# Kernel tuning notes

Hardware: AMD Instinct MI355X
Metric: run time of the kernel (lower is better)

The kernel has to match this reference:

```python
import jax, jax.numpy as jnp
import numpy as np
from jax import lax

B, HB, WB, CB = 128, 64, 64, 16      # board batch, height, width, channels
HI, WI, CI = 72, 72, 4               # image size/channels (fixed by module)
HIDC = CB - 4                         # board hidden channels = 12
IMGC = 72                             # img_channel_n
POSTC = IMGC + 4                      # 76
FIRE_RATE = 0.5
BN_EPS = 1e-3                         # keras BatchNormalization default epsilon


def setup_inputs() -> dict:
    key = jax.random.key(0)
    k = jax.random.split(key, 8)
    x = jax.random.normal(k[0], (B, HB, WB, CB), jnp.float32)
    images = jax.random.uniform(k[1], (B, HI, WI, CI), jnp.float32)
    conv1_w = jax.random.normal(k[2], (3, 3, CI, 32), jnp.float32) * (1.0 / np.sqrt(9 * CI))
    conv2_w = jax.random.normal(k[3], (3, 3, 32, 32), jnp.float32) * (1.0 / np.sqrt(9 * 32))
    flat = (HI // 4) * (WI // 4) * 32  # 18*18*32 = 10368 after two 2x2 pools
    dense_w = jax.random.normal(k[4], (flat, HIDC * IMGC), jnp.float32) * (1.0 / np.sqrt(flat))
    upd_w1 = jax.random.normal(k[5], (POSTC * 3, 128), jnp.float32) * (1.0 / np.sqrt(POSTC * 3))
    upd_w2 = jax.random.normal(k[6], (128, CB), jnp.float32) * 0.02
    return dict(
        x=x, images=images,
        bn1_gamma=jnp.ones((CI,), jnp.float32), bn1_beta=jnp.zeros((CI,), jnp.float32),
        bn1_mean=jnp.zeros((CI,), jnp.float32), bn1_var=jnp.ones((CI,), jnp.float32),
        conv1_w=conv1_w, conv1_b=jnp.zeros((32,), jnp.float32),
        bn2_gamma=jnp.ones((32,), jnp.float32), bn2_beta=jnp.zeros((32,), jnp.float32),
        bn2_mean=jnp.zeros((32,), jnp.float32), bn2_var=jnp.ones((32,), jnp.float32),
        conv2_w=conv2_w, conv2_b=jnp.zeros((32,), jnp.float32),
        dense_w=dense_w, dense_b=jnp.zeros((HIDC * IMGC,), jnp.float32),
        upd_w1=upd_w1, upd_b1=jnp.zeros((128,), jnp.float32),
        upd_w2=upd_w2, upd_b2=jnp.zeros((CB,), jnp.float32),
    )


def _bn(x, g, b, m, v):
    return (x - m) * lax.rsqrt(v + BN_EPS) * g + b


def _conv_same(x, w, b):
    return lax.conv_general_dilated(x, w, (1, 1), 'SAME',
                                    dimension_numbers=('NHWC', 'HWIO', 'NHWC')) + b


def _maxpool2(x):
    return lax.reduce_window(x, -jnp.inf, lax.max, (1, 2, 2, 1), (1, 2, 2, 1), 'VALID')


def _living_mask(x):
    alpha = x[..., 3:4]
    return lax.reduce_window(alpha, -jnp.inf, lax.max, (1, 3, 3, 1), (1, 1, 1, 1), 'SAME') > 0.1


def _perception_kernel(c):
    # identity + sobel-x + sobel-y, depthwise with multiplier 3 (channel-major order c*3+m)
    ident = np.zeros((3, 3), np.float32); ident[1, 1] = 1.0
    sx = (np.outer([1, 2, 1], [-1, 0, 1]) / 8.0).astype(np.float32)
    sy = sx.T
    k = np.stack([ident, sx, sy], -1)       # (3,3,3)
    k = np.tile(k, (1, 1, c))                # (3,3,3c)
    return jnp.asarray(k[:, :, None, :])     # HWIO with I=1, O=3c


def reference(x, images, bn1_gamma, bn1_beta, bn1_mean, bn1_var, conv1_w, conv1_b,
              bn2_gamma, bn2_beta, bn2_mean, bn2_var, conv2_w, conv2_b,
              dense_w, dense_b, upd_w1, upd_b1, upd_w2, upd_b2):
    # ---- image model (inference mode: BN uses moving stats, dropout = identity) ----
    h = _bn(images, bn1_gamma, bn1_beta, bn1_mean, bn1_var)
    h = jax.nn.relu(_conv_same(h, conv1_w, conv1_b))
    h = _maxpool2(h)
    h = _bn(h, bn2_gamma, bn2_beta, bn2_mean, bn2_var)
    h = jax.nn.relu(_conv_same(h, conv2_w, conv2_b))
    h = _maxpool2(h)
    h = h.reshape(h.shape[0], -1)
    h = jax.nn.relu(h @ dense_w + dense_b)
    filters = h.reshape(-1, HIDC, IMGC)      # (B, 12, 72): per-sample 1x1 conv filter

    # ---- CA step ----
    pre_life = _living_mask(x)
    board_out = x[..., :4]
    hidden = x[..., 4:]
    # per-batch 1x1 VALID conv == batched channel contraction
    img_conv = jnp.einsum('bhwc,bco->bhwo', hidden, filters)
    img_aware = jnp.concatenate([board_out, img_conv], axis=-1)   # (B,H,W,76)
    kern = _perception_kernel(POSTC)
    perceived = lax.conv_general_dilated(img_aware, kern, (1, 1), 'SAME',
                                         dimension_numbers=('NHWC', 'HWIO', 'NHWC'),
                                         feature_group_count=POSTC)  # (B,H,W,228)
    u = jax.nn.relu(jnp.einsum('bhwc,cd->bhwd', perceived, upd_w1) + upd_b1)
    dx = jnp.einsum('bhwd,de->bhwe', u, upd_w2) + upd_b2
    update_mask = jax.random.uniform(jax.random.key(42), x[..., :1].shape) <= FIRE_RATE
    x = x + dx * update_mask.astype(x.dtype)
    post_life = _living_mask(x)
    living = (pre_life & post_life).astype(x.dtype)
    return x * living
```

## Files before the change

### kernel.cpp

```cpp
#include <hip/hip_runtime.h>

#define BN_EPS 1e-3f

typedef __attribute__((ext_vector_type(8))) short bf16x8;
typedef __attribute__((ext_vector_type(4))) short s16x4;
typedef __attribute__((ext_vector_type(4))) float f32x4;

__device__ __forceinline__ unsigned short f2bf_rne(float f) {
  unsigned u = __float_as_uint(f);
  unsigned r = u + 0x7fffu + ((u >> 16) & 1u);
  return (unsigned short)(r >> 16);
}
__device__ __forceinline__ float bf2f(unsigned short h) {
  return __uint_as_float(((unsigned)h) << 16);
}
__device__ __forceinline__ void split2(float v, unsigned short& h, unsigned short& l) {
  h = f2bf_rne(v);
  l = f2bf_rne(v - bf2f(h));
}
__device__ __forceinline__ void split2t(float v, unsigned short& h, unsigned short& l) {
  unsigned u = __float_as_uint(v);
  float hi = __uint_as_float(u & 0xFFFF0000u);
  h = (unsigned short)(u >> 16);
  l = f2bf_rne(v - hi);
}

__device__ __forceinline__ unsigned rotl32(unsigned v, int n) {
  return (v << n) | (v >> (32 - n));
}

__device__ __forceinline__ float tf42_uniform(unsigned i) {
  unsigned x0 = 0u, x1 = i;
  const unsigned k0 = 0u, k1 = 42u, k2 = 0u ^ 42u ^ 0x1BD11BDAu;
  x0 += k0; x1 += k1;
#define TFR(r) { x0 += x1; x1 = rotl32(x1, r); x1 ^= x0; }
  TFR(13) TFR(15) TFR(26) TFR(6)
  x0 += k1; x1 += k2 + 1u;
  TFR(17) TFR(29) TFR(16) TFR(24)
  x0 += k2; x1 += k0 + 2u;
  TFR(13) TFR(15) TFR(26) TFR(6)
  x0 += k0; x1 += k1 + 3u;
  TFR(17) TFR(29) TFR(16) TFR(24)
  x0 += k1; x1 += k2 + 4u;
  TFR(13) TFR(15) TFR(26) TFR(6)
  x0 += k2; x1 += k0 + 5u;
#undef TFR
  unsigned bits = x0 ^ x1;
  return __uint_as_float((bits >> 9) | 0x3F800000u) - 1.0f;
}

__global__ __launch_bounds__(256) void k_conv1(
    const float* __restrict__ img,
    const float* __restrict__ g1, const float* __restrict__ be1,
    const float* __restrict__ m1, const float* __restrict__ v1,
    const float* __restrict__ w, const float* __restrict__ bias,
    const float* __restrict__ g2, const float* __restrict__ be2,
    const float* __restrict__ m2, const float* __restrict__ v2,
    float* __restrict__ h1) {
  int t = blockIdx.x * 256 + threadIdx.x;
  int ox = t % 36, oy = (t / 36) % 36, b = t / 1296;
  float s1[4], t1[4];
#pragma unroll
  for (int ci = 0; ci < 4; ++ci) {
    float s = g1[ci] / sqrtf(v1[ci] + BN_EPS);
    s1[ci] = s; t1[ci] = be1[ci] - m1[ci] * s;
  }
  float pacc[32];
#pragma unroll
  for (int co = 0; co < 32; ++co) pacc[co] = 0.f;
#pragma unroll
  for (int sy = 0; sy < 2; ++sy)
#pragma unroll
  for (int sx = 0; sx < 2; ++sx) {
    int iy = 2 * oy + sy, ix = 2 * ox + sx;
    float acc[32];
#pragma unroll
    for (int co = 0; co < 32; ++co) acc[co] = bias[co];
    for (int ky = 0; ky < 3; ++ky) {
      int yy = iy + ky - 1; if (yy < 0 || yy >= 72) continue;
      for (int kx = 0; kx < 3; ++kx) {
        int xx = ix + kx - 1; if (xx < 0 || xx >= 72) continue;
        float4 p = *(const float4*)(img + (((size_t)b * 72 + yy) * 72 + xx) * 4);
        float in0 = p.x * s1[0] + t1[0];
        float in1 = p.y * s1[1] + t1[1];
        float in2 = p.z * s1[2] + t1[2];
        float in3 = p.w * s1[3] + t1[3];
        const float* wp = w + (ky * 3 + kx) * 128;
#pragma unroll
        for (int co = 0; co < 32; ++co) acc[co] = fmaf(in0, wp[co], acc[co]);
#pragma unroll
        for (int co = 0; co < 32; ++co) acc[co] = fmaf(in1, wp[32 + co], acc[co]);
#pragma unroll
        for (int co = 0; co < 32; ++co) acc[co] = fmaf(in2, wp[64 + co], acc[co]);
#pragma unroll
        for (int co = 0; co < 32; ++co) acc[co] = fmaf(in3, wp[96 + co], acc[co]);
      }
    }
#pragma unroll
    for (int co = 0; co < 32; ++co)
      pacc[co] = fmaxf(pacc[co], fmaxf(acc[co], 0.f));
  }
#pragma unroll
  for (int co = 0; co < 32; ++co) {
    float s = g2[co] / sqrtf(v2[co] + BN_EPS);
    pacc[co] = pacc[co] * s + (be2[co] - m2[co] * s);
  }
  float* op = h1 + (size_t)t * 32;
#pragma unroll
  for (int c4 = 0; c4 < 8; ++c4) {
    float4 v;
    v.x = pacc[c4 * 4]; v.y = pacc[c4 * 4 + 1];
    v.z = pacc[c4 * 4 + 2]; v.w = pacc[c4 * 4 + 3];
    *(float4*)(op + c4 * 4) = v;
  }
}

__global__ __launch_bounds__(256) void k_prep3(
    const float* __restrict__ w, unsigned short* __restrict__ Wh,
    unsigned short* __restrict__ Wl) {
  int t = blockIdx.x * 256 + threadIdx.x;
  int j = t & 7, l = (t >> 3) & 63, nt = (t >> 9) & 1, tap = t >> 10;
  int ci = ((l >> 4) << 3) + j, co = nt * 16 + (l & 15);
  float v = w[tap * 1024 + ci * 32 + co];
  unsigned short hh, ll;
  split2(v, hh, ll);
  Wh[t] = hh;
  Wl[t] = ll;
}

__global__ __launch_bounds__(256, 3) void k_conv2(
    const float* __restrict__ hin,
    const unsigned short* __restrict__ Wch, const unsigned short* __restrict__ Wcl,
    const float* __restrict__ bias, float* __restrict__ h2) {
  __shared__ __align__(16) unsigned short Lh[12960];
  __shared__ __align__(16) unsigned short Ll[12960];
  int tid = threadIdx.x;
  int b = blockIdx.y;
  int tY = (blockIdx.x / 3) * 16, tX = (blockIdx.x % 3) * 16;
  for (int idx = tid; idx < 2592; idx += 256) {
    int pix = idx >> 3, c4 = idx & 7;
    int ly = pix / 18, lx = pix - ly * 18;
    int gy = tY - 1 + ly, gx = tX - 1 + lx;
    float4 v = {0.f, 0.f, 0.f, 0.f};
    if (gy >= 0 && gy < 36 && gx >= 0 && gx < 36)
      v = *(const float4*)(hin + (((size_t)b * 36 + gy) * 36 + gx) * 32 + c4 * 4);
    unsigned short ha, la, hb, lb, hc, lc, hd, ld;
    split2(v.x, ha, la); split2(v.y, hb, lb);
    split2(v.z, hc, lc); split2(v.w, hd, ld);
    s16x4 vh = {(short)ha, (short)hb, (short)hc, (short)hd};
    s16x4 vl = {(short)la, (short)lb, (short)lc, (short)ld};
    *(s16x4*)(Lh + pix * 40 + c4 * 4) = vh;
    *(s16x4*)(Ll + pix * 40 + c4 * 4) = vl;
  }
  __syncthreads();
  int wv = tid >> 6, lane = tid & 63;
  int lr = lane & 15, lhi = lane >> 4;
  int nt = wv & 1, mrow0 = (wv >> 1) * 8;
  bf16x8 wh[9], wl[9];
#pragma unroll
  for (int tap = 0; tap < 9; ++tap) {
    int base = ((tap * 2 + nt) * 64 + lane) * 8;
    wh[tap] = *(const bf16x8*)(Wch + base);
    wl[tap] = *(const bf16x8*)(Wcl + base);
  }
  f32x4 acc[8];
#pragma unroll
  for (int mt = 0; mt < 8; ++mt) acc[mt] = (f32x4){0.f, 0.f, 0.f, 0.f};
#pragma unroll
  for (int mt = 0; mt < 8; ++mt) {
    int row = mrow0 + mt;
#pragma unroll
    for (int tap = 0; tap < 9; ++tap) {
      int dy = tap / 3, dx = tap - dy * 3;
      int pixel = (row + dy) * 18 + (lr + dx);
      bf16x8 ah = *(const bf16x8*)(Lh + pixel * 40 + lhi * 8);
      bf16x8 al = *(const bf16x8*)(Ll + pixel * 40 + lhi * 8);
      acc[mt] = __builtin_amdgcn_mfma_f32_16x16x32_bf16(ah, wh[tap], acc[mt], 0, 0, 0);
      acc[mt] = __builtin_amdgcn_mfma_f32_16x16x32_bf16(ah, wl[tap], acc[mt], 0, 0, 0);
      acc[mt] = __builtin_amdgcn_mfma_f32_16x16x32_bf16(al, wh[tap], acc[mt], 0, 0, 0);
    }
  }
  int co = nt * 16 + lr;
  float bv = bias[co];
#pragma unroll
  for (int a = 0; a < 4; ++a) {
#pragma unroll
    for (int bb = 0; bb < 2; ++bb) {
      float v00 = fmaxf(acc[2 * a][2 * bb] + bv, 0.f);
      float v01 = fmaxf(acc[2 * a][2 * bb + 1] + bv, 0.f);
      float v10 = fmaxf(acc[2 * a + 1][2 * bb] + bv, 0.f);
      float v11 = fmaxf(acc[2 * a + 1][2 * bb + 1] + bv, 0.f);
      float p = fmaxf(fmaxf(v00, v01), fmaxf(v10, v11));
      int gy = (tY >> 1) + (mrow0 >> 1) + a;
      int gx = (tX >> 1) + lhi * 2 + bb;
      if (gy < 18 && gx < 18)
        h2[(((size_t)b * 18 + gy) * 18 + gx) * 32 + co] = p;
    }
  }
}

__global__ __launch_bounds__(256) void k_dense_part(
    const float* __restrict__ h2, const float* __restrict__ w,
    float* __restrict__ part) {
  __shared__ __align__(16) unsigned short Ah[128 * 40];
  __shared__ __align__(16) unsigned short Al[128 * 40];
  __shared__ __align__(16) unsigned short Bh[64 * 40];
  __shared__ __align__(16) unsigned short Bl[64 * 40];
  int tid = threadIdx.x;
  int n0 = blockIdx.x * 64;
  int kc = blockIdx.y;
  int wv = tid >> 6, lane = tid & 63;
  int lr = lane & 15, lhi = lane >> 4;
  f32x4 acc[8];
#pragma unroll
  for (int m = 0; m < 8; ++m) acc[m] = (f32x4){0.f, 0.f, 0.f, 0.f};
  for (int kt = 0; kt < 18; ++kt) {
    int kb = kc * 576 + kt * 32;
    if (kt) __syncthreads();
#pragma unroll
    for (int it = 0; it < 4; ++it) {
      int f = tid + it * 256;
      int ml = f >> 3, kq = f & 7;
      float4 p = *(const float4*)(h2 + (size_t)ml * 10368 + kb + kq * 4);
      unsigned short h0, l0, h1, l1, h2_, l2_, h3, l3;
      split2t(p.x, h0, l0); split2t(p.y, h1, l1);
      split2t(p.z, h2_, l2_); split2t(p.w, h3, l3);
      s16x4 vh = {(short)h0, (short)h1, (short)h2_, (short)h3};
      s16x4 vl = {(short)l0, (short)l1, (short)l2_, (short)l3};
      *(s16x4*)(Ah + ml * 40 + kq * 4) = vh;
      *(s16x4*)(Al + ml * 40 + kq * 4) = vl;
    }
#pragma unroll
    for (int it = 0; it < 2; ++it) {
      int f = tid + it * 256;
      int kr = f >> 4, n4 = (f & 15) * 4;
      float4 p = {0.f, 0.f, 0.f, 0.f};
      if (n0 + n4 < 864)
        p = *(const float4*)(w + (size_t)(kb + kr) * 864 + n0 + n4);
      unsigned short hh, ll;
      split2t(p.x, hh, ll); Bh[(n4 + 0) * 40 + kr] = hh; Bl[(n4 + 0) * 40 + kr] = ll;
      split2t(p.y, hh, ll); Bh[(n4 + 1) * 40 + kr] = hh; Bl[(n4 + 1) * 40 + kr] = ll;
      split2t(p.z, hh, ll); Bh[(n4 + 2) * 40 + kr] = hh; Bl[(n4 + 2) * 40 + kr] = ll;
      split2t(p.w, hh, ll); Bh[(n4 + 3) * 40 + kr] = hh; Bl[(n4 + 3) * 40 + kr] = ll;
    }
    __syncthreads();
    bf16x8 bh_ = *(const bf16x8*)(Bh + (wv * 16 + lr) * 40 + lhi * 8);
    bf16x8 bl_ = *(const bf16x8*)(Bl + (wv * 16 + lr) * 40 + lhi * 8);
#pragma unroll
    for (int m = 0; m < 8; ++m) {
      bf16x8 ah = *(const bf16x8*)(Ah + (m * 16 + lr) * 40 + lhi * 8);
      bf16x8 al = *(const bf16x8*)(Al + (m * 16 + lr) * 40 + lhi * 8);
      acc[m] = __builtin_amdgcn_mfma_f32_16x16x32_bf16(ah, bh_, acc[m], 0, 0, 0);
      acc[m] = __builtin_amdgcn_mfma_f32_16x16x32_bf16(ah, bl_, acc[m], 0, 0, 0);
      acc[m] = __builtin_amdgcn_mfma_f32_16x16x32_bf16(al, bh_, acc[m], 0, 0, 0);
    }
  }
  int n = n0 + wv * 16 + lr;
  if (n < 864) {
#pragma unroll
    for (int m = 0; m < 8; ++m) {
#pragma unroll
      for (int r = 0; r < 4; ++r) {
        int mm = m * 16 + lhi * 4 + r;
        part[((size_t)kc * 128 + mm) * 864 + n] = acc[m][r];
      }
    }
  }
}

__global__ __launch_bounds__(256) void k_dense_fin(
    const float* __restrict__ part, const float* __restrict__ bias,
    float* __restrict__ filt) {
  int e = blockIdx.x * 256 + threadIdx.x;
  float s = bias[e % 864];
#pragma unroll
  for (int kc = 0; kc < 18; ++kc) s += part[(size_t)kc * 110592 + e];
  filt[e] = fmaxf(s, 0.f);
}

__global__ __launch_bounds__(256) void k_prep2(
    const float* __restrict__ filt, const float* __restrict__ W1,
    const float* __restrict__ W2,
    unsigned short* __restrict__ Eh, unsigned short* __restrict__ El,
    unsigned short* __restrict__ W2h, unsigned short* __restrict__ W2l) {
  __shared__ float fl[864];
  int b = blockIdx.x;
  int tid = threadIdx.x;
  if (b == 128) {
    for (int t = tid; t < 2048; t += 256) {
      int j = t & 7, l = (t >> 3) & 63, ks = t >> 9;
      int k = 32 * ks + ((l >> 4) << 3) + j;
      int col = l & 15;
      float v = W2[k * 16 + col];
      unsigned short hh, ll;
      split2(v, hh, ll);
      W2h[t] = hh;
      W2l[t] = ll;
    }
    return;
  }
  for (int f = tid; f < 864; f += 256) fl[f] = filt[(size_t)b * 864 + f];
  __syncthreads();
  int col = tid & 127;
  int k0 = tid >> 7;
  for (int k = k0; k < 64; k += 2) {
    float v;
    if (k < 12) {
      v = W1[k * 128 + col];
    } else if (k < 48) {
      int h = (k - 12) / 3, t = (k - 12) % 3;
      const float* wp = W1 + (12 + t) * 128 + col;
      const float* fp = fl + h * 72;
      float a0 = 0.f, a1 = 0.f, a2 = 0.f, a3 = 0.f;
      for (int c = 0; c < 72; c += 4) {
        a0 = fmaf(fp[c], wp[(size_t)c * 384], a0);
        a1 = fmaf(fp[c + 1], wp[(size_t)(c + 1) * 384], a1);
        a2 = fmaf(fp[c + 2], wp[(size_t)(c + 2) * 384], a2);
        a3 = fmaf(fp[c + 3], wp[(size_t)(c + 3) * 384], a3);
      }
      v = (a0 + a1) + (a2 + a3);
    } else {
      v = 0.f;
    }
    unsigned short hh, ll;
    split2(v, hh, ll);
    int ks = k >> 5, j = k & 7, a4 = (k >> 3) & 3;
    int l = a4 * 16 + (col & 15), nt = col >> 4;
    size_t o = (((size_t)b * 8 + nt) * 2 + ks) * 512 + l * 8 + j;
    Eh[o] = hh;
    El[o] = ll;
  }
}

__global__ __launch_bounds__(256, 4) void k_ca(
    const float* __restrict__ x,
    const unsigned short* __restrict__ Eh, const unsigned short* __restrict__ El,
    const float* __restrict__ B1,
    const unsigned short* __restrict__ W2h, const unsigned short* __restrict__ W2l,
    const float* __restrict__ B2,
    float* __restrict__ xnew, float* __restrict__ aold,
    float* __restrict__ anew) {
  __shared__ __align__(16) unsigned char S[35072];
  float* ia = (float*)S;
  unsigned short* PAh = (unsigned short*)(S + 7680);
  unsigned short* PAl = (unsigned short*)(S + 16896);
  unsigned short* Uh = (unsigned short*)S;
  unsigned short* Ul = (unsigned short*)(S + 17408);
  float* mskL = (float*)(S + 34816);

  int tid = threadIdx.x;
  int b = blockIdx.y;
  int tx = (blockIdx.x & 7) * 8, ty = (blockIdx.x >> 3) * 8;
  int wv = tid >> 6, lane = tid & 63;
  int lr = lane & 15, lhi = lane >> 4;

  bf16x8 bh[2][2], bl[2][2];
#pragma unroll
  for (int nt = 0; nt < 2; ++nt)
#pragma unroll
    for (int ks = 0; ks < 2; ++ks) {
      size_t base = (((size_t)b * 8 + (wv * 2 + nt)) * 2 + ks) * 512 + lane * 8;
      bh[nt][ks] = *(const bf16x8*)(Eh + base);
      bl[nt][ks] = *(const bf16x8*)(El + base);
    }
  float xo[4];
#pragma unroll
  for (int r = 0; r < 4; ++r) {
    int px = wv * 16 + lhi * 4 + r;
    int gy = ty + (px >> 3), gx = tx + (px & 7);
    xo[r] = x[(((size_t)b * 64 + gy) * 64 + gx) * 16 + lr];
  }

  if (tid < 200) {
    int px_ = tid >> 1, half = tid & 1;
    int hy = px_ / 10, hx = px_ - hy * 10;
    int pp = hy * 12 + hx;
    int gy = ty + hy - 1, gx = tx + hx - 1;
    float4 v0 = {0.f, 0.f, 0.f, 0.f}, v1 = {0.f, 0.f, 0.f, 0.f};
    if (gy >= 0 && gy < 64 && gx >= 0 && gx < 64) {
      const float* xp = x + (((size_t)b * 64 + gy) * 64 + gx) * 16 + half * 8;
      v0 = *(const float4*)xp;
      v1 = *(const float4*)(xp + 4);
    }
    int c0 = half * 8;
    ia[(c0 + 0) * 120 + pp] = v0.x; ia[(c0 + 1) * 120 + pp] = v0.y;
    ia[(c0 + 2) * 120 + pp] = v0.z; ia[(c0 + 3) * 120 + pp] = v0.w;
    ia[(c0 + 4) * 120 + pp] = v1.x; ia[(c0 + 5) * 120 + pp] = v1.y;
    ia[(c0 + 6) * 120 + pp] = v1.z; ia[(c0 + 7) * 120 + pp] = v1.w;
  }
  {
    if (tid >= 192) {
      int p = tid - 192;
      int gy = ty + (p >> 3), gx = tx + (p & 7);
      unsigned pix = (unsigned)(b * 4096 + gy * 64 + gx);
      mskL[p] = (tf42_uniform(pix) <= 0.5f) ? 1.f : 0.f;
    }
    const s16x4 z4 = {0, 0, 0, 0};
    if (wv == 2) {
#pragma unroll
      for (int g = 0; g < 4; ++g) *(s16x4*)(PAh + lane * 72 + 48 + 4 * g) = z4;
    }
    if (wv == 3) {
#pragma unroll
      for (int g = 0; g < 4; ++g) *(s16x4*)(PAl + lane * 72 + 48 + 4 * g) = z4;
    }
  }
  __syncthreads();

  {
    int py = lane >> 3, pxx = lane & 7;
    const float* pc0 = ia + (py + 1) * 12 + (pxx + 1);
    unsigned short oh[12], ol[12];
#pragma unroll
    for (int i = 0; i < 4; ++i) {
      const float* pc = pc0 + (wv * 4 + i) * 120;
      float n00 = pc[-13], n01 = pc[-12], n02 = pc[-11];
      float n10 = pc[-1],  n11 = pc[0],   n12 = pc[1];
      float n20 = pc[11],  n21 = pc[12],  n22 = pc[13];
      float pid = n11;
      float psx = ((n02 - n00) + 2.f * (n12 - n10) + (n22 - n20)) * 0.125f;
      float psy = ((n20 - n00) + 2.f * (n21 - n01) + (n22 - n02)) * 0.125f;
      split2(pid, oh[3 * i + 0], ol[3 * i + 0]);
      split2(psx, oh[3 * i + 1], ol[3 * i + 1]);
      split2(psy, oh[3 * i + 2], ol[3 * i + 2]);
    }
    int off = lane * 72 + wv * 12;
#pragma unroll
    for (int g = 0; g < 3; ++g) {
      s16x4 vh = {(short)oh[4 * g], (short)oh[4 * g + 1],
                  (short)oh[4 * g + 2], (short)oh[4 * g + 3]};
      s16x4 vl = {(short)ol[4 * g], (short)ol[4 * g + 1],
                  (short)ol[4 * g + 2], (short)ol[4 * g + 3]};
      *(s16x4*)(PAh + off + 4 * g) = vh;
      *(s16x4*)(PAl + off + 4 * g) = vl;
    }
  }
  __syncthreads();

  f32x4 acc[4][2];
#pragma unroll
  for (int m = 0; m < 4; ++m)
#pragma unroll
    for (int nt = 0; nt < 2; ++nt)
      acc[m][nt] = (f32x4){0.f, 0.f, 0.f, 0.f};
#pragma unroll
  for (int ks = 0; ks < 2; ++ks) {
#pragma unroll
    for (int m = 0; m < 4; ++m) {
      int arow = m * 16 + lr;
      bf16x8 pah = *(const bf16x8*)(PAh + arow * 72 + ks * 32 + lhi * 8);
      bf16x8 pal = *(const bf16x8*)(PAl + arow * 72 + ks * 32 + lhi * 8);
#pragma unroll
      for (int nt = 0; nt < 2; ++nt) {
        acc[m][nt] = __builtin_amdgcn_mfma_f32_16x16x32_bf16(
            pah, bh[nt][ks], acc[m][nt], 0, 0, 0);
        acc[m][nt] = __builtin_amdgcn_mfma_f32_16x16x32_bf16(
            pah, bl[nt][ks], acc[m][nt], 0, 0, 0);
        acc[m][nt] = __builtin_amdgcn_mfma_f32_16x16x32_bf16(
            pal, bh[nt][ks], acc[m][nt], 0, 0, 0);
      }
    }
  }
  bf16x8 ch_[4], cl_[4];
#pragma unroll
  for (int ks = 0; ks < 4; ++ks) {
    ch_[ks] = *(const bf16x8*)(W2h + ks * 512 + lane * 8);
    cl_[ks] = *(const bf16x8*)(W2l + ks * 512 + lane * 8);
  }
  __syncthreads();

  int d0 = wv * 32;
  float b1v0 = B1[d0 + lr], b1v1 = B1[d0 + 16 + lr];
#pragma unroll
  for (int m = 0; m < 4; ++m)
#pragma unroll
    for (int nt = 0; nt < 2; ++nt) {
      float bv = nt ? b1v1 : b1v0;
      int hid = d0 + nt * 16 + lr;
#pragma unroll
      for (int r = 0; r < 4; ++r) {
        int px = m * 16 + lhi * 4 + r;
        float uval = fmaxf(acc[m][nt][r] + bv, 0.f);
        unsigned short hh, ll;
        split2(uval, hh, ll);
        Uh[px * 136 + hid] = hh;
        Ul[px * 136 + hid] = ll;
      }
    }
  __syncthreads();

  f32x4 acc2 = {0.f, 0.f, 0.f, 0.f};
#pragma unroll
  for (int ks = 0; ks < 4; ++ks) {
    bf16x8 uh_ = *(const bf16x8*)(Uh + (wv * 16 + lr) * 136 + ks * 32 + lhi * 8);
    bf16x8 ul_ = *(const bf16x8*)(Ul + (wv * 16 + lr) * 136 + ks * 32 + lhi * 8);
    acc2 = __builtin_amdgcn_mfma_f32_16x16x32_bf16(uh_, ch_[ks], acc2, 0, 0, 0);
    acc2 = __builtin_amdgcn_mfma_f32_16x16x32_bf16(uh_, cl_[ks], acc2, 0, 0, 0);
    acc2 = __builtin_amdgcn_mfma_f32_16x16x32_bf16(ul_, ch_[ks], acc2, 0, 0, 0);
  }

  float b2v = B2[lr];
#pragma unroll
  for (int r = 0; r < 4; ++r) {
    int px = wv * 16 + lhi * 4 + r;
    int gy = ty + (px >> 3), gx = tx + (px & 7);
    float m_ = mskL[px];
    float xn = xo[r] + (acc2[r] + b2v) * m_;
    size_t o = (((size_t)b * 64 + gy) * 64 + gx) * 16 + lr;
    xnew[o] = xn;
    if (lr == 3) {
      unsigned pix = (unsigned)(b * 4096 + gy * 64 + gx);
      aold[pix] = xo[r];
      anew[pix] = xn;
    }
  }
}

__global__ __launch_bounds__(256) void k_final(
    float* __restrict__ xnew, const float* __restrict__ aold,
    const float* __restrict__ anew) {
  int t = blockIdx.x * 256 + threadIdx.x;
  int gx = t & 63, gy = (t >> 6) & 63, b = t >> 12;
  float mo = -1e30f, mn = -1e30f;
  for (int dy = -1; dy <= 1; ++dy) {
    int yy = gy + dy; if (yy < 0 || yy >= 64) continue;
    for (int dx = -1; dx <= 1; ++dx) {
      int xx = gx + dx; if (xx < 0 || xx >= 64) continue;
      int p = b * 4096 + yy * 64 + xx;
      mo = fmaxf(mo, aold[p]);
      mn = fmaxf(mn, anew[p]);
    }
  }
  float live = (mo > 0.1f && mn > 0.1f) ? 1.f : 0.f;
  size_t base = (size_t)t * 16;
#pragma unroll
  for (int c4 = 0; c4 < 4; ++c4) {
    float4 v = *(const float4*)(xnew + base + c4 * 4);
    v.x *= live; v.y *= live; v.z *= live; v.w *= live;
    *(float4*)(xnew + base + c4 * 4) = v;
  }
}

extern "C" void kernel_launch(void* const* d_in, const int* in_sizes, int n_in,
                              void* d_out, int out_size, void* d_ws, size_t ws_size,
                              hipStream_t stream) {
  const float* x    = (const float*)d_in[0];
  const float* img  = (const float*)d_in[1];
  const float* g1   = (const float*)d_in[2];
  const float* be1  = (const float*)d_in[3];
  const float* m1   = (const float*)d_in[4];
  const float* v1   = (const float*)d_in[5];
  const float* w1c  = (const float*)d_in[6];
  const float* b1c  = (const float*)d_in[7];
  const float* g2   = (const float*)d_in[8];
  const float* be2  = (const float*)d_in[9];
  const float* m2   = (const float*)d_in[10];
  const float* v2   = (const float*)d_in[11];
  const float* w2c  = (const float*)d_in[12];
  const float* b2c  = (const float*)d_in[13];
  const float* dw   = (const float*)d_in[14];
  const float* db   = (const float*)d_in[15];
  const float* uw1  = (const float*)d_in[16];
  const float* ub1  = (const float*)d_in[17];
  const float* uw2  = (const float*)d_in[18];
  const float* ub2  = (const float*)d_in[19];

  char* ws = (char*)d_ws;
  float* h1   = (float*)(ws);
  float* part = h1;
  float* h2   = (float*)(ws + 21233664);
  float* filt = (float*)(ws + 26542080);
  float* aold = (float*)(ws + 26984448);
  float* anew = (float*)(ws + 29081600);
  unsigned short* W2Bh = (unsigned short*)(ws + 31178752);
  unsigned short* W2Bl = (unsigned short*)(ws + 31182848);
  unsigned short* Wc2h = (unsigned short*)(ws + 31186944);
  unsigned short* Wc2l = (unsigned short*)(ws + 31205376);
  unsigned short* W1Eh = (unsigned short*)(ws);
  unsigned short* W1El = (unsigned short*)(ws + 2097152);
  float* xnew = (float*)d_out;

  k_prep3<<<36, 256, 0, stream>>>(w2c, Wc2h, Wc2l);
  k_conv1<<<648, 256, 0, stream>>>(img, g1, be1, m1, v1, w1c, b1c,
                                   g2, be2, m2, v2, h1);
  k_conv2<<<dim3(9, 128), 256, 0, stream>>>(h1, Wc2h, Wc2l, b2c, h2);
  k_dense_part<<<dim3(14, 18), 256, 0, stream>>>(h2, dw, part);
  k_dense_fin<<<432, 256, 0, stream>>>(part, db, filt);
  k_prep2<<<129, 256, 0, stream>>>(filt, uw1, uw2, W1Eh, W1El, W2Bh, W2Bl);
  k_ca<<<dim3(64, 128), 256, 0, stream>>>(x, W1Eh, W1El, ub1, W2Bh, W2Bl, ub2,
                                          xnew, aold, anew);
  k_final<<<2048, 256, 0, stream>>>(xnew, aold, anew);
}
```

Baseline: 201.2 us.

## Move conv1 onto bf16 MFMA with split-precision tiles and fused pool

```diff
diff --git a/kernel.cpp b/kernel.cpp
--- a/kernel.cpp
+++ b/kernel.cpp
@@ -49,69 +49,110 @@
   return __uint_as_float((bits >> 9) | 0x3F800000u) - 1.0f;
 }
 
+__global__ __launch_bounds__(256) void k_prep4(
+    const float* __restrict__ w, unsigned short* __restrict__ Wh,
+    unsigned short* __restrict__ Wl) {
+  int t = blockIdx.x * 256 + threadIdx.x;
+  int j = t & 7, l = (t >> 3) & 63, nt = (t >> 9) & 1, ks = t >> 10;
+  int k = 32 * ks + ((l >> 4) << 3) + j;
+  int tap = k >> 3, ci = k & 7;
+  float v = (tap < 9 && ci < 4) ? w[tap * 128 + ci * 32 + nt * 16 + (l & 15)] : 0.f;
+  unsigned short hh, ll;
+  split2(v, hh, ll);
+  Wh[t] = hh;
+  Wl[t] = ll;
+}
+
 __global__ __launch_bounds__(256) void k_conv1(
     const float* __restrict__ img,
     const float* __restrict__ g1, const float* __restrict__ be1,
     const float* __restrict__ m1, const float* __restrict__ v1,
-    const float* __restrict__ w, const float* __restrict__ bias,
+    const unsigned short* __restrict__ Wc1h, const unsigned short* __restrict__ Wc1l,
+    const float* __restrict__ bias,
     const float* __restrict__ g2, const float* __restrict__ be2,
     const float* __restrict__ m2, const float* __restrict__ v2,
     float* __restrict__ h1) {
-  int t = blockIdx.x * 256 + threadIdx.x;
-  int ox = t % 36, oy = (t / 36) % 36, b = t / 1296;
+  __shared__ __align__(16) unsigned short Lh[2592];
+  __shared__ __align__(16) unsigned short Ll[2592];
+  int tid = threadIdx.x;
+  int b = blockIdx.y;
+  int tY = (blockIdx.x / 5) * 16, tX = (blockIdx.x % 5) * 16;
   float s1[4], t1[4];
 #pragma unroll
   for (int ci = 0; ci < 4; ++ci) {
     float s = g1[ci] / sqrtf(v1[ci] + BN_EPS);
     s1[ci] = s; t1[ci] = be1[ci] - m1[ci] * s;
   }
-  float pacc[32];
-#pragma unroll
-  for (int co = 0; co < 32; ++co) pacc[co] = 0.f;
-#pragma unroll
-  for (int sy = 0; sy < 2; ++sy)
-#pragma unroll
-  for (int sx = 0; sx < 2; ++sx) {
-    int iy = 2 * oy + sy, ix = 2 * ox + sx;
-    float acc[32];
-#pragma unroll
-    for (int co = 0; co < 32; ++co) acc[co] = bias[co];
-    for (int ky = 0; ky < 3; ++ky) {
-      int yy = iy + ky - 1; if (yy < 0 || yy >= 72) continue;
-      for (int kx = 0; kx < 3; ++kx) {
-        int xx = ix + kx - 1; if (xx < 0 || xx >= 72) continue;
-        float4 p = *(const float4*)(img + (((size_t)b * 72 + yy) * 72 + xx) * 4);
-        float in0 = p.x * s1[0] + t1[0];
-        float in1 = p.y * s1[1] + t1[1];
-        float in2 = p.z * s1[2] + t1[2];
-        float in3 = p.w * s1[3] + t1[3];
-        const float* wp = w + (ky * 3 + kx) * 128;
-#pragma unroll
-        for (int co = 0; co < 32; ++co) acc[co] = fmaf(in0, wp[co], acc[co]);
-#pragma unroll
-        for (int co = 0; co < 32; ++co) acc[co] = fmaf(in1, wp[32 + co], acc[co]);
-#pragma unroll
-        for (int co = 0; co < 32; ++co) acc[co] = fmaf(in2, wp[64 + co], acc[co]);
-#pragma unroll
-        for (int co = 0; co < 32; ++co) acc[co] = fmaf(in3, wp[96 + co], acc[co]);
-      }
-    }
-#pragma unroll
-    for (int co = 0; co < 32; ++co)
-      pacc[co] = fmaxf(pacc[co], fmaxf(acc[co], 0.f));
-  }
-#pragma unroll
-  for (int co = 0; co < 32; ++co) {
-    float s = g2[co] / sqrtf(v2[co] + BN_EPS);
-    pacc[co] = pacc[co] * s + (be2[co] - m2[co] * s);
-  }
-  float* op = h1 + (size_t)t * 32;
-#pragma unroll
-  for (int c4 = 0; c4 < 8; ++c4) {
-    float4 v;
-    v.x = pacc[c4 * 4]; v.y = pacc[c4 * 4 + 1];
-    v.z = pacc[c4 * 4 + 2]; v.w = pacc[c4 * 4 + 3];
-    *(float4*)(op + c4 * 4) = v;
+  const s16x4 z4 = {0, 0, 0, 0};
+  for (int idx = tid; idx < 324; idx += 256) {
+    int ly = idx / 18, lx = idx - ly * 18;
+    int gy = tY - 1 + ly, gx = tX - 1 + lx;
+    float4 v = {0.f, 0.f, 0.f, 0.f};
+    if (gy >= 0 && gy < 72 && gx >= 0 && gx < 72) {
+      v = *(const float4*)(img + (((size_t)b * 72 + gy) * 72 + gx) * 4);
+      v.x = v.x * s1[0] + t1[0];
+      v.y = v.y * s1[1] + t1[1];
+      v.z = v.z * s1[2] + t1[2];
+      v.w = v.w * s1[3] + t1[3];
+    }
+    unsigned short ha, la, hb, lb, hc, lc, hd, ld;
+    split2t(v.x, ha, la); split2t(v.y, hb, lb);
+    split2t(v.z, hc, lc); split2t(v.w, hd, ld);
+    s16x4 vh = {(short)ha, (short)hb, (short)hc, (short)hd};
+    s16x4 vl = {(short)la, (short)lb, (short)lc, (short)ld};
+    *(s16x4*)(Lh + idx * 8) = vh;
+    *(s16x4*)(Lh + idx * 8 + 4) = z4;
+    *(s16x4*)(Ll + idx * 8) = vl;
+    *(s16x4*)(Ll + idx * 8 + 4) = z4;
+  }
+  __syncthreads();
+  int wv = tid >> 6, lane = tid & 63;
+  int lr = lane & 15, lhi = lane >> 4;
+  int nt = wv & 1, mrow0 = (wv >> 1) * 8;
+  bf16x8 wh[3], wl[3];
+#pragma unroll
+  for (int ks = 0; ks < 3; ++ks) {
+    int base = ((ks * 2 + nt) * 64 + lane) * 8;
+    wh[ks] = *(const bf16x8*)(Wc1h + base);
+    wl[ks] = *(const bf16x8*)(Wc1l + base);
+  }
+  f32x4 acc[8];
+#pragma unroll
+  for (int mt = 0; mt < 8; ++mt) acc[mt] = (f32x4){0.f, 0.f, 0.f, 0.f};
+#pragma unroll
+  for (int ks = 0; ks < 3; ++ks) {
+    int tap = 4 * ks + lhi;
+    int tc = tap > 8 ? 8 : tap;
+    int dy = tc / 3, dx = tc - 3 * dy;
+#pragma unroll
+    for (int mt = 0; mt < 8; ++mt) {
+      int row = mrow0 + mt;
+      int px = (row + dy) * 18 + lr + dx;
+      bf16x8 ah = *(const bf16x8*)(Lh + px * 8);
+      bf16x8 al = *(const bf16x8*)(Ll + px * 8);
+      acc[mt] = __builtin_amdgcn_mfma_f32_16x16x32_bf16(ah, wh[ks], acc[mt], 0, 0, 0);
+      acc[mt] = __builtin_amdgcn_mfma_f32_16x16x32_bf16(ah, wl[ks], acc[mt], 0, 0, 0);
+      acc[mt] = __builtin_amdgcn_mfma_f32_16x16x32_bf16(al, wh[ks], acc[mt], 0, 0, 0);
+    }
+  }
+  int co = nt * 16 + lr;
+  float bv = bias[co];
+  float s2 = g2[co] / sqrtf(v2[co] + BN_EPS);
+  float t2 = be2[co] - m2[co] * s2;
+#pragma unroll
+  for (int a = 0; a < 4; ++a) {
+#pragma unroll
+    for (int bb = 0; bb < 2; ++bb) {
+      float v00 = fmaxf(acc[2 * a][2 * bb] + bv, 0.f);
+      float v01 = fmaxf(acc[2 * a][2 * bb + 1] + bv, 0.f);
+      float v10 = fmaxf(acc[2 * a + 1][2 * bb] + bv, 0.f);
+      float v11 = fmaxf(acc[2 * a + 1][2 * bb + 1] + bv, 0.f);
+      float p = fmaxf(fmaxf(v00, v01), fmaxf(v10, v11));
+      int gy = (tY >> 1) + (mrow0 >> 1) + a;
+      int gx = (tX >> 1) + lhi * 2 + bb;
+      if (gy < 36 && gx < 36)
+        h1[(((size_t)b * 36 + gy) * 36 + gx) * 32 + co] = p * s2 + t2;
+    }
   }
 }
 
@@ -145,8 +186,8 @@
     if (gy >= 0 && gy < 36 && gx >= 0 && gx < 36)
       v = *(const float4*)(hin + (((size_t)b * 36 + gy) * 36 + gx) * 32 + c4 * 4);
     unsigned short ha, la, hb, lb, hc, lc, hd, ld;
-    split2(v.x, ha, la); split2(v.y, hb, lb);
-    split2(v.z, hc, lc); split2(v.w, hd, ld);
+    split2t(v.x, ha, la); split2t(v.y, hb, lb);
+    split2t(v.z, hc, lc); split2t(v.w, hd, ld);
     s16x4 vh = {(short)ha, (short)hb, (short)hc, (short)hd};
     s16x4 vl = {(short)la, (short)lb, (short)lc, (short)ld};
     *(s16x4*)(Lh + pix * 40 + c4 * 4) = vh;
@@ -420,9 +461,9 @@
       float pid = n11;
       float psx = ((n02 - n00) + 2.f * (n12 - n10) + (n22 - n20)) * 0.125f;
       float psy = ((n20 - n00) + 2.f * (n21 - n01) + (n22 - n02)) * 0.125f;
-      split2(pid, oh[3 * i + 0], ol[3 * i + 0]);
-      split2(psx, oh[3 * i + 1], ol[3 * i + 1]);
-      split2(psy, oh[3 * i + 2], ol[3 * i + 2]);
+      split2t(pid, oh[3 * i + 0], ol[3 * i + 0]);
+      split2t(psx, oh[3 * i + 1], ol[3 * i + 1]);
+      split2t(psy, oh[3 * i + 2], ol[3 * i + 2]);
     }
     int off = lane * 72 + wv * 12;
 #pragma unroll
@@ -482,7 +523,7 @@
         int px = m * 16 + lhi * 4 + r;
         float uval = fmaxf(acc[m][nt][r] + bv, 0.f);
         unsigned short hh, ll;
-        split2(uval, hh, ll);
+        split2t(uval, hh, ll);
         Uh[px * 136 + hid] = hh;
         Ul[px * 136 + hid] = ll;
       }
@@ -576,13 +617,16 @@
   unsigned short* W2Bl = (unsigned short*)(ws + 31182848);
   unsigned short* Wc2h = (unsigned short*)(ws + 31186944);
   unsigned short* Wc2l = (unsigned short*)(ws + 31205376);
+  unsigned short* Wc1h = (unsigned short*)(ws + 31223808);
+  unsigned short* Wc1l = (unsigned short*)(ws + 31229952);
   unsigned short* W1Eh = (unsigned short*)(ws);
   unsigned short* W1El = (unsigned short*)(ws + 2097152);
   float* xnew = (float*)d_out;
 
+  k_prep4<<<12, 256, 0, stream>>>(w1c, Wc1h, Wc1l);
   k_prep3<<<36, 256, 0, stream>>>(w2c, Wc2h, Wc2l);
-  k_conv1<<<648, 256, 0, stream>>>(img, g1, be1, m1, v1, w1c, b1c,
-                                   g2, be2, m2, v2, h1);
+  k_conv1<<<dim3(25, 128), 256, 0, stream>>>(img, g1, be1, m1, v1, Wc1h, Wc1l,
+                                             b1c, g2, be2, m2, v2, h1);
   k_conv2<<<dim3(9, 128), 256, 0, stream>>>(h1, Wc2h, Wc2l, b2c, h2);
   k_dense_part<<<dim3(14, 18), 256, 0, stream>>>(h2, dw, part);
   k_dense_fin<<<432, 256, 0, stream>>>(part, db, filt);
```

Result: faster. 181.4 us (-9.8%).
